# Kernel tuning notes

Measured on AMD Instinct MI355X. Metric: run time of the kernel, lower is better.

The kernel has to match this reference:

```python
import jax, jax.numpy as jnp
import numpy as np

B, S, E, H, V, C = 256, 20, 512, 512, 32000, 1000


def _lstm_step(x, h, c, W, U, b):
    # Keras LSTM, activation='relu', recurrent_activation='sigmoid', gate order i,f,c,o
    z = x @ W + h @ U + b  # (B, 4H)
    i, f, g, o = jnp.split(z, 4, axis=-1)
    i = jax.nn.sigmoid(i)
    f = jax.nn.sigmoid(f)
    g = jax.nn.relu(g)
    o = jax.nn.sigmoid(o)
    c_new = f * c + i * g
    h_new = o * jax.nn.relu(c_new)
    return h_new, c_new


def setup_inputs() -> dict:
    key = jax.random.key(0)
    ks = jax.random.split(key, 24)
    std = 0.05
    d_in1 = S * E + 2 * E  # flattened encoder output + word embed + speaker embed
    inp = {
        "encoded_output": jax.random.normal(ks[0], (B, S, E), jnp.float32),
        "word_embedding": jax.random.normal(ks[1], (B, E), jnp.float32),
        "h0": jax.random.normal(ks[2], (B, H), jnp.float32) * std,
        "c0": jax.random.normal(ks[3], (B, H), jnp.float32) * std,
        "speaker": jax.random.randint(ks[4], (B,), 0, C),
        "addressee": jax.random.randint(ks[5], (B,), 0, C),
        "persona_emb": jax.random.normal(ks[6], (C, E), jnp.float32) * 0.1,
        "W1": jax.random.normal(ks[7], (d_in1, 4 * H), jnp.float32) * std,
        "U1": jax.random.normal(ks[8], (H, 4 * H), jnp.float32) * std,
        "b1": jnp.zeros((4 * H,), jnp.float32),
        "W2": jax.random.normal(ks[9], (H, 4 * H), jnp.float32) * std,
        "U2": jax.random.normal(ks[10], (H, 4 * H), jnp.float32) * std,
        "b2": jnp.zeros((4 * H,), jnp.float32),
        "W3": jax.random.normal(ks[11], (H, 4 * H), jnp.float32) * std,
        "U3": jax.random.normal(ks[12], (H, 4 * H), jnp.float32) * std,
        "b3": jnp.zeros((4 * H,), jnp.float32),
        "W4": jax.random.normal(ks[13], (H, 4 * H), jnp.float32) * std,
        "U4": jax.random.normal(ks[14], (H, 4 * H), jnp.float32) * std,
        "b4": jnp.zeros((4 * H,), jnp.float32),
        "Wd": jax.random.normal(ks[15], (H, V), jnp.float32) * std,
        "bd": jnp.zeros((V,), jnp.float32),
    }
    return inp


def reference(encoded_output, word_embedding, h0, c0, speaker, addressee,
              persona_emb, W1, U1, b1, W2, U2, b2, W3, U3, b3, W4, U4, b4, Wd, bd):
    b = encoded_output.shape[0]
    # The Python double loop in the original is exactly: (B,S,E) -> (B, S*E)
    enc_flat = encoded_output.reshape(b, -1)
    speaker_embed = persona_emb[speaker]  # (B, E)
    # is_speaker=True branch: concat [flattened encoder, word embed, speaker embed]
    x = jnp.concatenate([enc_flat, word_embedding, speaker_embed], axis=-1)
    # seq length is 1, so each LSTM layer is a single cell step;
    # each layer's initial state is the previous layer's final (h, c)
    h1, c1 = _lstm_step(x, h0, c0, W1, U1, b1)
    h2, c2 = _lstm_step(h1, h1, c1, W2, U2, b2)
    h3, c3 = _lstm_step(h2, h2, c2, W3, U3, b3)
    h4, c4 = _lstm_step(h3, h3, c3, W4, U4, b4)
    probs = jax.nn.softmax(h4 @ Wd + bd, axis=-1)  # (B, V)
    return probs, (h4, c4)
```

## Files before the change

kernel.cpp:

```cpp
#include <hip/hip_runtime.h>
#include <cstdint>
#include <cmath>

typedef _Float16 f16;
typedef _Float16 f16x8 __attribute__((ext_vector_type(8)));
typedef float f32x4 __attribute__((ext_vector_type(4)));

__device__ inline void gld_lds16(const void* g, void* l) {
  __builtin_amdgcn_global_load_lds(
      (__attribute__((address_space(1))) void*)(uintptr_t)g,
      (__attribute__((address_space(3))) void*)l, 16, 0, 0);
}

__global__ __launch_bounds__(256) void build_x1_kernel(
    const float* __restrict__ enc, const float* __restrict__ word,
    const float* __restrict__ pers, const int* __restrict__ speaker,
    const float* __restrict__ h0, f16* __restrict__ X)
{
  const int b  = blockIdx.y;
  const int k2 = blockIdx.x * 256 + threadIdx.x;
  const int k  = k2 * 2;
  float v0, v1;
  if (k < 10240) {
    const float* p = enc + (long long)b * 10240 + k; v0 = p[0]; v1 = p[1];
  } else if (k < 10752) {
    const float* p = word + b * 512 + (k - 10240);   v0 = p[0]; v1 = p[1];
  } else if (k < 11264) {
    const float* p = pers + (long long)speaker[b] * 512 + (k - 10752); v0 = p[0]; v1 = p[1];
  } else {
    const float* p = h0 + b * 512 + (k - 11264);     v0 = p[0]; v1 = p[1];
  }
  union { f16 h[2]; unsigned int u; } pk;
  pk.h[0] = (f16)v0; pk.h[1] = (f16)v1;
  ((unsigned int*)X)[(long long)b * 5888 + k2] = pk.u;
}

__global__ __launch_bounds__(256, 2) void gemm_f16_kernel(
    const f16* __restrict__ A, int lda, int a_kmask,
    const float* __restrict__ B0, const float* __restrict__ B1, int ksw, int ldb,
    float* __restrict__ C, int ldc, long long c_split_stride, int kchunk)
{
  __shared__ __align__(16) f16 Ah[128 * 32];
  __shared__ __align__(16) f16 Bh[128 * 40];

  const int tid  = threadIdx.x;
  const int lane = tid & 63;
  const int wave = tid >> 6;
  const int m0 = blockIdx.x * 128;
  const int n0 = blockIdx.y * 128;
  const int kbeg = blockIdx.z * kchunk;
  const int kend = kbeg + kchunk;
  float* Cs = C + (long long)blockIdx.z * c_split_stride;

  const int wm = (wave & 1) * 64;
  const int wn = (wave >> 1) * 64;

  f32x4 acc[4][4] = {};

  const int a_row16 = lane >> 2;
  const int a_ksub  = (((lane & 3) ^ ((lane >> 3) & 3))) * 8;

  const int bk  = tid >> 3;
  const int bkc = bk >> 3;
  const int bkr = bk & 7;
  const int bn_base = (tid & 7) * 16;

  for (int kt = kbeg; kt < kend; kt += 32) {
    const int akb = kt & a_kmask;
    #pragma unroll
    for (int half = 0; half < 2; half++) {
      const int rb = wave * 32 + half * 16;
      const f16* gp = A + (long long)(m0 + rb + a_row16) * lda + akb + a_ksub;
      gld_lds16((const void*)gp, (void*)&Ah[rb * 32]);
    }
    {
      const int krow = kt + bk;
      const float* bp = (krow >= ksw) ? (B1 + (long long)(krow - ksw) * ldb)
                                      : (B0 + (long long)krow * ldb);
      bp += n0 + bn_base;
      #pragma unroll
      for (int j = 0; j < 4; j++) {
        const float4 v = *(const float4*)(bp + j * 4);
        const float vv[4] = {v.x, v.y, v.z, v.w};
        #pragma unroll
        for (int e = 0; e < 4; e++) {
          const int n = bn_base + j * 4 + e;
          Bh[n * 40 + ((bkc ^ ((n >> 4) & 3)) * 8) + bkr] = (f16)vv[e];
        }
      }
    }
    __syncthreads();

    f16x8 af[4], bf[4];
    #pragma unroll
    for (int mi = 0; mi < 4; mi++) {
      const int m = wm + mi * 16 + (lane & 15);
      const int c = (lane >> 4) ^ ((m >> 1) & 3);
      af[mi] = *(const f16x8*)&Ah[m * 32 + c * 8];
    }
    #pragma unroll
    for (int ni = 0; ni < 4; ni++) {
      const int n = wn + ni * 16 + (lane & 15);
      const int c = (lane >> 4) ^ ((n >> 4) & 3);
      bf[ni] = *(const f16x8*)&Bh[n * 40 + c * 8];
    }
    #pragma unroll
    for (int mi = 0; mi < 4; mi++)
      #pragma unroll
      for (int ni = 0; ni < 4; ni++)
        acc[mi][ni] = __builtin_amdgcn_mfma_f32_16x16x32_f16(af[mi], bf[ni], acc[mi][ni], 0, 0, 0);
    __syncthreads();
  }

  #pragma unroll
  for (int mi = 0; mi < 4; mi++) {
    const int r0 = m0 + wm + mi * 16 + (lane >> 4) * 4;
    #pragma unroll
    for (int ni = 0; ni < 4; ni++) {
      const int cc = n0 + wn + ni * 16 + (lane & 15);
      #pragma unroll
      for (int r = 0; r < 4; r++)
        Cs[(long long)(r0 + r) * ldc + cc] = acc[mi][ni][r];
    }
  }
}

__global__ __launch_bounds__(256) void gate_kernel(
    const float* __restrict__ zbase, int nsplit, const float* __restrict__ bias,
    const float* __restrict__ c_prev, float* __restrict__ c_out,
    f16* __restrict__ h16_out, float* __restrict__ h32_out)
{
  const int idx = blockIdx.x * 256 + threadIdx.x;
  const int j = idx & 511;
  const int b = idx >> 9;
  const long long zo = (long long)b * 2048 + j;
  float zi = bias[j], zf = bias[j + 512], zg = bias[j + 1024], zo4 = bias[j + 1536];
  for (int s = 0; s < nsplit; s++) {
    const float* z = zbase + (long long)s * 524288;
    zi += z[zo]; zf += z[zo + 512]; zg += z[zo + 1024]; zo4 += z[zo + 1536];
  }
  const float gi = 1.f / (1.f + expf(-zi));
  const float gf = 1.f / (1.f + expf(-zf));
  const float gg = fmaxf(zg, 0.f);
  const float go = 1.f / (1.f + expf(-zo4));
  const float cn = gf * c_prev[idx] + gi * gg;
  const float hn = go * fmaxf(cn, 0.f);
  c_out[idx] = cn;
  h16_out[idx] = (f16)hn;
  if (h32_out) h32_out[idx] = hn;
}

__global__ __launch_bounds__(1024) void softmax_kernel(
    float* __restrict__ logits, const float* __restrict__ bd)
{
  const int row = blockIdx.x;
  const int t = threadIdx.x;
  float* rp = logits + (long long)row * 32000;
  float l[32];
  float m = -1e30f;
  #pragma unroll
  for (int i = 0; i < 32; i++) {
    const int v = t + i * 1024;
    if (v < 32000) { l[i] = rp[v] + bd[v]; m = fmaxf(m, l[i]); }
    else l[i] = -1e30f;
  }
  #pragma unroll
  for (int off = 32; off > 0; off >>= 1) m = fmaxf(m, __shfl_xor(m, off, 64));
  __shared__ float redm[16];
  __shared__ float reds[16];
  const int w = t >> 6;
  if ((t & 63) == 0) redm[w] = m;
  __syncthreads();
  float bm = redm[0];
  #pragma unroll
  for (int i = 1; i < 16; i++) bm = fmaxf(bm, redm[i]);
  float s = 0.f;
  #pragma unroll
  for (int i = 0; i < 32; i++) {
    const float e = expf(l[i] - bm);
    l[i] = e;
    s += e;
  }
  #pragma unroll
  for (int off = 32; off > 0; off >>= 1) s += __shfl_xor(s, off, 64);
  if ((t & 63) == 0) reds[w] = s;
  __syncthreads();
  float ts = 0.f;
  #pragma unroll
  for (int i = 0; i < 16; i++) ts += reds[i];
  const float inv = 1.0f / ts;
  #pragma unroll
  for (int i = 0; i < 32; i++) {
    const int v = t + i * 1024;
    if (v < 32000) rp[v] = l[i] * inv;
  }
}

extern "C" void kernel_launch(void* const* d_in, const int* in_sizes, int n_in,
                              void* d_out, int out_size, void* d_ws, size_t ws_size,
                              hipStream_t stream) {
  const float* enc     = (const float*)d_in[0];
  const float* word    = (const float*)d_in[1];
  const float* h0      = (const float*)d_in[2];
  const float* c0      = (const float*)d_in[3];
  const int*   speaker = (const int*)d_in[4];
  const float* pers = (const float*)d_in[6];
  const float* W1 = (const float*)d_in[7];
  const float* U1 = (const float*)d_in[8];
  const float* b1 = (const float*)d_in[9];
  const float* W2 = (const float*)d_in[10];
  const float* U2 = (const float*)d_in[11];
  const float* b2 = (const float*)d_in[12];
  const float* W3 = (const float*)d_in[13];
  const float* U3 = (const float*)d_in[14];
  const float* b3 = (const float*)d_in[15];
  const float* W4 = (const float*)d_in[16];
  const float* U4 = (const float*)d_in[17];
  const float* b4 = (const float*)d_in[18];
  const float* Wd = (const float*)d_in[19];
  const float* bd = (const float*)d_in[20];

  float* out = (float*)d_out;
  float* zpart = out;
  f16*   X1h   = (f16*)((char*)d_out + 16777216);
  float* h4_out = out + 8192000;
  float* c4_out = out + 8192000 + 131072;

  float* ws_c   = (float*)d_ws;
  f16*   ws_h16 = (f16*)((char*)d_ws + 524288);

  const int BIG = 1 << 29;

  build_x1_kernel<<<dim3(23, 256), 256, 0, stream>>>(enc, word, pers, speaker, h0, X1h);

  gemm_f16_kernel<<<dim3(2, 16, 8), 256, 0, stream>>>(
      X1h, 11776, 0x7fffffff, W1, U1, 11264, 2048, zpart, 2048, 524288LL, 1472);
  gate_kernel<<<dim3(512), 256, 0, stream>>>(zpart, 8, b1, c0, ws_c, ws_h16, nullptr);

  gemm_f16_kernel<<<dim3(2, 16, 4), 256, 0, stream>>>(
      ws_h16, 512, 511, W2, U2, 512, 2048, zpart, 2048, 524288LL, 256);
  gate_kernel<<<dim3(512), 256, 0, stream>>>(zpart, 4, b2, ws_c, ws_c, ws_h16, nullptr);

  gemm_f16_kernel<<<dim3(2, 16, 4), 256, 0, stream>>>(
      ws_h16, 512, 511, W3, U3, 512, 2048, zpart, 2048, 524288LL, 256);
  gate_kernel<<<dim3(512), 256, 0, stream>>>(zpart, 4, b3, ws_c, ws_c, ws_h16, nullptr);

  gemm_f16_kernel<<<dim3(2, 16, 4), 256, 0, stream>>>(
      ws_h16, 512, 511, W4, U4, 512, 2048, zpart, 2048, 524288LL, 256);
  gate_kernel<<<dim3(512), 256, 0, stream>>>(zpart, 4, b4, ws_c, c4_out, ws_h16, h4_out);

  gemm_f16_kernel<<<dim3(2, 250, 1), 256, 0, stream>>>(
      ws_h16, 512, 0x7fffffff, Wd, Wd, BIG, 32000, out, 32000, 0LL, 512);

  softmax_kernel<<<dim3(256), 1024, 0, stream>>>(out, bd);
}
```

Baseline: 377.8 us.

## Halve GEMM N-tile, restructure B staging, raise split-K, vectorize softmax

The GEMM block tile shrinks from 128x128 to 128x64, with occupancy raised to 4 blocks per SM. B is now staged by having each thread load 8 consecutive k-rows of one column and write a packed f16x8 to LDS, replacing the scattered per-element writes. The grids double along N, and the LSTM layers 2-4 use 8-way split-K instead of 4-way, to put more blocks on the GPU for this memory-bound weight streaming. Softmax now uses float4 loads and stores. The trade-offs are more partial-sum traffic, A tiles reloaded by twice as many blocks, and B global reads that are 4-byte per thread across 8 rows rather than float4.

```diff
diff --git a/kernel.cpp b/kernel.cpp
--- a/kernel.cpp
+++ b/kernel.cpp
@@ -35,35 +35,33 @@
   ((unsigned int*)X)[(long long)b * 5888 + k2] = pk.u;
 }
 
-__global__ __launch_bounds__(256, 2) void gemm_f16_kernel(
+__global__ __launch_bounds__(256, 4) void gemm_f16_kernel(
     const f16* __restrict__ A, int lda, int a_kmask,
     const float* __restrict__ B0, const float* __restrict__ B1, int ksw, int ldb,
     float* __restrict__ C, int ldc, long long c_split_stride, int kchunk)
 {
   __shared__ __align__(16) f16 Ah[128 * 32];
-  __shared__ __align__(16) f16 Bh[128 * 40];
+  __shared__ __align__(16) f16 Bh[64 * 40];
 
   const int tid  = threadIdx.x;
   const int lane = tid & 63;
   const int wave = tid >> 6;
   const int m0 = blockIdx.x * 128;
-  const int n0 = blockIdx.y * 128;
+  const int n0 = blockIdx.y * 64;
   const int kbeg = blockIdx.z * kchunk;
   const int kend = kbeg + kchunk;
   float* Cs = C + (long long)blockIdx.z * c_split_stride;
 
   const int wm = (wave & 1) * 64;
-  const int wn = (wave >> 1) * 64;
-
-  f32x4 acc[4][4] = {};
+  const int wn = (wave >> 1) * 32;
+
+  f32x4 acc[4][2] = {};
 
   const int a_row16 = lane >> 2;
-  const int a_ksub  = (((lane & 3) ^ ((lane >> 3) & 3))) * 8;
-
-  const int bk  = tid >> 3;
-  const int bkc = bk >> 3;
-  const int bkr = bk & 7;
-  const int bn_base = (tid & 7) * 16;
+  const int a_ksub  = ((lane & 3) ^ ((lane >> 3) & 3)) * 8;
+
+  const int bn  = tid & 63;
+  const int boct = tid >> 6;
 
   for (int kt = kbeg; kt < kend; kt += 32) {
     const int akb = kt & a_kmask;
@@ -74,24 +72,22 @@
       gld_lds16((const void*)gp, (void*)&Ah[rb * 32]);
     }
     {
-      const int krow = kt + bk;
-      const float* bp = (krow >= ksw) ? (B1 + (long long)(krow - ksw) * ldb)
-                                      : (B0 + (long long)krow * ldb);
-      bp += n0 + bn_base;
-      #pragma unroll
-      for (int j = 0; j < 4; j++) {
-        const float4 v = *(const float4*)(bp + j * 4);
-        const float vv[4] = {v.x, v.y, v.z, v.w};
-        #pragma unroll
-        for (int e = 0; e < 4; e++) {
-          const int n = bn_base + j * 4 + e;
-          Bh[n * 40 + ((bkc ^ ((n >> 4) & 3)) * 8) + bkr] = (f16)vv[e];
-        }
+      float bv[8];
+      #pragma unroll
+      for (int i = 0; i < 8; i++) {
+        const int krow = kt + boct * 8 + i;
+        const float* bp = (krow >= ksw) ? (B1 + (long long)(krow - ksw) * ldb)
+                                        : (B0 + (long long)krow * ldb);
+        bv[i] = bp[n0 + bn];
       }
+      f16x8 pk;
+      #pragma unroll
+      for (int i = 0; i < 8; i++) pk[i] = (f16)bv[i];
+      *(f16x8*)&Bh[bn * 40 + boct * 8] = pk;
     }
     __syncthreads();
 
-    f16x8 af[4], bf[4];
+    f16x8 af[4], bf[2];
     #pragma unroll
     for (int mi = 0; mi < 4; mi++) {
       const int m = wm + mi * 16 + (lane & 15);
@@ -99,15 +95,14 @@
       af[mi] = *(const f16x8*)&Ah[m * 32 + c * 8];
     }
     #pragma unroll
-    for (int ni = 0; ni < 4; ni++) {
+    for (int ni = 0; ni < 2; ni++) {
       const int n = wn + ni * 16 + (lane & 15);
-      const int c = (lane >> 4) ^ ((n >> 4) & 3);
-      bf[ni] = *(const f16x8*)&Bh[n * 40 + c * 8];
+      bf[ni] = *(const f16x8*)&Bh[n * 40 + (lane >> 4) * 8];
     }
     #pragma unroll
     for (int mi = 0; mi < 4; mi++)
       #pragma unroll
-      for (int ni = 0; ni < 4; ni++)
+      for (int ni = 0; ni < 2; ni++)
         acc[mi][ni] = __builtin_amdgcn_mfma_f32_16x16x32_f16(af[mi], bf[ni], acc[mi][ni], 0, 0, 0);
     __syncthreads();
   }
@@ -116,7 +111,7 @@
   for (int mi = 0; mi < 4; mi++) {
     const int r0 = m0 + wm + mi * 16 + (lane >> 4) * 4;
     #pragma unroll
-    for (int ni = 0; ni < 4; ni++) {
+    for (int ni = 0; ni < 2; ni++) {
       const int cc = n0 + wn + ni * 16 + (lane & 15);
       #pragma unroll
       for (int r = 0; r < 4; r++)
@@ -155,14 +150,21 @@
 {
   const int row = blockIdx.x;
   const int t = threadIdx.x;
-  float* rp = logits + (long long)row * 32000;
-  float l[32];
+  float4* rp = (float4*)(logits + (long long)row * 32000);
+  const float4* bp = (const float4*)bd;
+  float4 l[8];
   float m = -1e30f;
   #pragma unroll
-  for (int i = 0; i < 32; i++) {
+  for (int i = 0; i < 8; i++) {
     const int v = t + i * 1024;
-    if (v < 32000) { l[i] = rp[v] + bd[v]; m = fmaxf(m, l[i]); }
-    else l[i] = -1e30f;
+    if (v < 8000) {
+      float4 x = rp[v]; const float4 bb = bp[v];
+      x.x += bb.x; x.y += bb.y; x.z += bb.z; x.w += bb.w;
+      l[i] = x;
+      m = fmaxf(m, fmaxf(fmaxf(x.x, x.y), fmaxf(x.z, x.w)));
+    } else {
+      l[i] = make_float4(-1e30f, -1e30f, -1e30f, -1e30f);
+    }
   }
   #pragma unroll
   for (int off = 32; off > 0; off >>= 1) m = fmaxf(m, __shfl_xor(m, off, 64));
@@ -176,10 +178,11 @@
   for (int i = 1; i < 16; i++) bm = fmaxf(bm, redm[i]);
   float s = 0.f;
   #pragma unroll
-  for (int i = 0; i < 32; i++) {
-    const float e = expf(l[i] - bm);
-    l[i] = e;
-    s += e;
+  for (int i = 0; i < 8; i++) {
+    const float ex = expf(l[i].x - bm), ey = expf(l[i].y - bm);
+    const float ez = expf(l[i].z - bm), ew = expf(l[i].w - bm);
+    l[i] = make_float4(ex, ey, ez, ew);
+    s += (ex + ey) + (ez + ew);
   }
   #pragma unroll
   for (int off = 32; off > 0; off >>= 1) s += __shfl_xor(s, off, 64);
@@ -190,9 +193,13 @@
   for (int i = 0; i < 16; i++) ts += reds[i];
   const float inv = 1.0f / ts;
   #pragma unroll
-  for (int i = 0; i < 32; i++) {
+  for (int i = 0; i < 8; i++) {
     const int v = t + i * 1024;
-    if (v < 32000) rp[v] = l[i] * inv;
+    if (v < 8000) {
+      float4 x = l[i];
+      x.x *= inv; x.y *= inv; x.z *= inv; x.w *= inv;
+      rp[v] = x;
+    }
   }
 }
 
@@ -233,23 +240,23 @@
 
   build_x1_kernel<<<dim3(23, 256), 256, 0, stream>>>(enc, word, pers, speaker, h0, X1h);
 
-  gemm_f16_kernel<<<dim3(2, 16, 8), 256, 0, stream>>>(
+  gemm_f16_kernel<<<dim3(2, 32, 8), 256, 0, stream>>>(
       X1h, 11776, 0x7fffffff, W1, U1, 11264, 2048, zpart, 2048, 524288LL, 1472);
   gate_kernel<<<dim3(512), 256, 0, stream>>>(zpart, 8, b1, c0, ws_c, ws_h16, nullptr);
 
-  gemm_f16_kernel<<<dim3(2, 16, 4), 256, 0, stream>>>(
-      ws_h16, 512, 511, W2, U2, 512, 2048, zpart, 2048, 524288LL, 256);
-  gate_kernel<<<dim3(512), 256, 0, stream>>>(zpart, 4, b2, ws_c, ws_c, ws_h16, nullptr);
-
-  gemm_f16_kernel<<<dim3(2, 16, 4), 256, 0, stream>>>(
-      ws_h16, 512, 511, W3, U3, 512, 2048, zpart, 2048, 524288LL, 256);
-  gate_kernel<<<dim3(512), 256, 0, stream>>>(zpart, 4, b3, ws_c, ws_c, ws_h16, nullptr);
-
-  gemm_f16_kernel<<<dim3(2, 16, 4), 256, 0, stream>>>(
-      ws_h16, 512, 511, W4, U4, 512, 2048, zpart, 2048, 524288LL, 256);
-  gate_kernel<<<dim3(512), 256, 0, stream>>>(zpart, 4, b4, ws_c, c4_out, ws_h16, h4_out);
-
-  gemm_f16_kernel<<<dim3(2, 250, 1), 256, 0, stream>>>(
+  gemm_f16_kernel<<<dim3(2, 32, 8), 256, 0, stream>>>(
+      ws_h16, 512, 511, W2, U2, 512, 2048, zpart, 2048, 524288LL, 128);
+  gate_kernel<<<dim3(512), 256, 0, stream>>>(zpart, 8, b2, ws_c, ws_c, ws_h16, nullptr);
+
+  gemm_f16_kernel<<<dim3(2, 32, 8), 256, 0, stream>>>(
+      ws_h16, 512, 511, W3, U3, 512, 2048, zpart, 2048, 524288LL, 128);
+  gate_kernel<<<dim3(512), 256, 0, stream>>>(zpart, 8, b3, ws_c, ws_c, ws_h16, nullptr);
+
+  gemm_f16_kernel<<<dim3(2, 32, 8), 256, 0, stream>>>(
+      ws_h16, 512, 511, W4, U4, 512, 2048, zpart, 2048, 524288LL, 128);
+  gate_kernel<<<dim3(512), 256, 0, stream>>>(zpart, 8, b4, ws_c, c4_out, ws_h16, h4_out);
+
+  gemm_f16_kernel<<<dim3(2, 500, 1), 256, 0, stream>>>(
       ws_h16, 512, 0x7fffffff, Wd, Wd, BIG, 32000, out, 32000, 0LL, 512);
 
   softmax_kernel<<<dim3(256), 1024, 0, stream>>>(out, bd);
```

After: 389.4 us. 3.1% more time.
